# Performance work log

Hardware: AMD Instinct MI355X
Metric: run time of the kernel (lower is better)

The kernel has to match this reference:

```python
import jax, jax.numpy as jnp
import numpy as np

B, L, D = 64, 192, 1024        # batch, tokens (pre_len), in_dim
RES, DIFF, COND = 512, 256, 512
H, DH = 16, 64                 # heads, dim_head; inner = H*DH = 1024
INNER = H * DH
DFF = 4 * D                    # LinearEncoder d_ff
LC = 192                       # cond length


def setup_inputs() -> dict:
    key = jax.random.key(0)
    ks = jax.random.split(key, 16)
    n = lambda k, s, sc=1.0: jax.random.normal(k, s, dtype=jnp.float32) * sc
    return {
        "x": n(ks[0], (B, L, D)),
        "conds": n(ks[1], (B, LC, COND)),
        "diff_emb": n(ks[2], (B, DIFF)),
        "w_diff": n(ks[3], (2 * RES, DIFF), 0.02), "b_diff": jnp.zeros((2 * RES,), jnp.float32),
        "w_cond": n(ks[4], (2 * RES, COND), 0.02), "b_cond": jnp.zeros((2 * RES,), jnp.float32),
        "wq": n(ks[5], (INNER, D), 0.02),
        "wk": n(ks[6], (INNER, 2 * RES), 0.02),
        "wv": n(ks[7], (INNER, 2 * RES), 0.02),
        "wo": n(ks[8], (D, INNER), 0.02), "bo": jnp.zeros((D,), jnp.float32),
        "ln1_g": jnp.ones((D,), jnp.float32), "ln1_b": jnp.zeros((D,), jnp.float32),
        "ln2_g": jnp.ones((D,), jnp.float32), "ln2_b": jnp.zeros((D,), jnp.float32),
        "w_out": n(ks[9], (2 * D, RES), 0.02), "b_out": jnp.zeros((2 * D,), jnp.float32),
        "enc_wv": n(ks[10], (D, D), 0.02), "enc_bv": jnp.zeros((D,), jnp.float32),
        "enc_wo": n(ks[11], (D, D), 0.02), "enc_bo": jnp.zeros((D,), jnp.float32),
        "weight_mat": (jnp.eye(L, dtype=jnp.float32) + jax.random.normal(ks[12], (L, L), dtype=jnp.float32))[None],
        "conv1_w": n(ks[13], (DFF, D), 0.02), "conv1_b": jnp.zeros((DFF,), jnp.float32),
        "conv2_w": n(ks[14], (D, DFF), 0.02), "conv2_b": jnp.zeros((D,), jnp.float32),
        "enc_n1_g": jnp.ones((D,), jnp.float32), "enc_n1_b": jnp.zeros((D,), jnp.float32),
        "enc_n2_g": jnp.ones((D,), jnp.float32), "enc_n2_b": jnp.zeros((D,), jnp.float32),
    }


def _ln(x, g, b):
    m = jnp.mean(x, -1, keepdims=True)
    v = jnp.mean((x - m) ** 2, -1, keepdims=True)
    return (x - m) * jax.lax.rsqrt(v + 1e-5) * g + b


def reference(x, conds, diff_emb, w_diff, b_diff, w_cond, b_cond, wq, wk, wv, wo, bo,
              ln1_g, ln1_b, ln2_g, ln2_b, w_out, b_out, enc_wv, enc_bv, enc_wo, enc_bo,
              weight_mat, conv1_w, conv1_b, conv2_w, conv2_b,
              enc_n1_g, enc_n1_b, enc_n2_g, enc_n2_b):
    res = x
    # diff embedding broadcast-add (permute/unsqueeze in torch == add over token dim)
    x = x + (diff_emb @ w_diff.T + b_diff)[:, None, :]          # [B,L,D]
    # --- LinearEncoder (dropout is identity at inference) ---
    values = x @ enc_wv.T + enc_bv
    A = jax.nn.softplus(weight_mat[0])                          # [L,L]
    A = A / jnp.sum(A, -1, keepdims=True)                       # F.normalize(p=1)
    new_x = jnp.einsum('ij,bjd->bid', A, values)                # token mixing
    x = x + new_x @ enc_wo.T + enc_bo
    x = _ln(x, enc_n1_g, enc_n1_b)
    y = jax.nn.gelu(jnp.einsum('bld,fd->blf', x, conv1_w) + conv1_b, approximate=False)
    y = jnp.einsum('blf,df->bld', y, conv2_w) + conv2_b
    x = _ln(x + y, enc_n2_g, enc_n2_b)
    # --- norm1 + cross attention ---
    x = _ln(x, ln1_g, ln1_b)
    cond = conds @ w_cond.T + b_cond                            # [B,Lc,2*RES]
    b, l = x.shape[0], x.shape[1]
    q = (x @ wq.T).reshape(b, l, H, DH)
    k = (cond @ wk.T).reshape(b, -1, H, DH)
    v = (cond @ wv.T).reshape(b, -1, H, DH)
    scale = DH ** -0.5
    sim = jnp.einsum('bihd,bjhd->bhij', q * scale, k)           # [B,H,L,Lc]
    attn = jax.nn.softmax(sim, axis=-1)
    o = jnp.einsum('bhij,bjhd->bihd', attn, v).reshape(b, l, INNER)
    x = o @ wo.T + bo
    # --- gated residual ---
    x = _ln(x, ln2_g, ln2_b)
    gate, filt = jnp.split(x, 2, axis=2)
    x = jnp.tanh(gate) * jax.nn.sigmoid(filt)                   # [B,L,RES]
    x = x @ w_out.T + b_out                                     # [B,L,2D]
    x = jnp.where(x >= 0, x, 0.4 * x)                           # leaky_relu(0.4)
    out, skip = jnp.split(x, 2, axis=2)
    out = (res + out) / jnp.sqrt(jnp.float32(2.0))
    return out, skip
```

## Files before the change

### kernel.cpp

```cpp
#include <hip/hip_runtime.h>

typedef unsigned short ushort_t;
typedef __attribute__((ext_vector_type(8))) short bf16x8;
typedef __attribute__((ext_vector_type(4))) float f32x4;
typedef __attribute__((ext_vector_type(4))) unsigned short u16x4;

#define DEV __device__ __forceinline__

typedef const __attribute__((address_space(1))) void GV;
typedef __attribute__((address_space(3))) void SV;

DEV void gl_lds16(const ushort_t* g, ushort_t* l) {
    __builtin_amdgcn_global_load_lds((GV*)g, (SV*)l, 16, 0, 0);
}

DEV float bf2f(unsigned short u) {
    union { unsigned u; float f; } c; c.u = ((unsigned)u) << 16; return c.f;
}
DEV unsigned short f2bf(float f) {
    union { float f; unsigned u; } c; c.f = f;
    unsigned u = c.u + 0x7fffu + ((c.u >> 16) & 1u);
    return (unsigned short)(u >> 16);
}

DEV f32x4 mfma32(bf16x8 a, bf16x8 b, f32x4 c) {
    return __builtin_amdgcn_mfma_f32_16x16x32_bf16(a, b, c, 0, 0, 0);
}

#define VMCNT6  asm volatile("s_waitcnt vmcnt(6)" ::: "memory")
#define VMCNT0  asm volatile("s_waitcnt vmcnt(0)" ::: "memory")
#define LGKM0   asm volatile("s_waitcnt lgkmcnt(0)" ::: "memory")
#define SCHEDB  __builtin_amdgcn_sched_barrier(0)
#define BAR     __builtin_amdgcn_s_barrier()

struct CvtSeg { const float* src; ushort_t* dst; };
struct CvtArgs { CvtSeg s[10]; int cum[11]; };

__global__ void cvt_multi(CvtArgs a, int total4) {
    for (int i = blockIdx.x * 256 + threadIdx.x; i < total4; i += gridDim.x * 256) {
        int seg = 0;
        #pragma unroll
        for (int t = 1; t < 10; t++) if (i >= a.cum[t]) seg = t;
        int off = i - a.cum[seg];
        f32x4 v = *(const f32x4*)(a.s[seg].src + (size_t)off * 4);
        u16x4 o;
        #pragma unroll
        for (int j = 0; j < 4; j++) o[j] = f2bf(v[j]);
        *(u16x4*)(a.s[seg].dst + (size_t)off * 4) = o;
    }
}

__global__ void cvt_kernel(const float* __restrict__ in, ushort_t* __restrict__ out, int n4) {
    for (int i = blockIdx.x * 256 + threadIdx.x; i < n4; i += gridDim.x * 256) {
        f32x4 v = *(const f32x4*)(in + (size_t)i * 4);
        u16x4 o;
        #pragma unroll
        for (int j = 0; j < 4; j++) o[j] = f2bf(v[j]);
        *(u16x4*)(out + (size_t)i * 4) = o;
    }
}

__global__ void anorm_kernel(const float* __restrict__ wm, ushort_t* __restrict__ apad) {
    int row = blockIdx.x;
    int lane = threadIdx.x;
    if (row >= 192) {
        apad[row * 192 + lane] = 0;
        apad[row * 192 + lane + 64] = 0;
        apad[row * 192 + lane + 128] = 0;
        return;
    }
    float x0 = wm[row * 192 + lane];
    float x1 = wm[row * 192 + lane + 64];
    float x2 = wm[row * 192 + lane + 128];
    float s0 = (x0 > 20.f) ? x0 : log1pf(expf(x0));
    float s1 = (x1 > 20.f) ? x1 : log1pf(expf(x1));
    float s2 = (x2 > 20.f) ? x2 : log1pf(expf(x2));
    float t = s0 + s1 + s2;
    #pragma unroll
    for (int m = 1; m < 64; m <<= 1) t += __shfl_xor(t, m);
    float inv = 1.f / t;
    apad[row * 192 + lane]       = f2bf(s0 * inv);
    apad[row * 192 + lane + 64]  = f2bf(s1 * inv);
    apad[row * 192 + lane + 128] = f2bf(s2 * inv);
}

__global__ void diffproj_kernel(const float* __restrict__ emb, const float* __restrict__ w,
                                const float* __restrict__ bias, float* __restrict__ out) {
    int id = blockIdx.x * 256 + threadIdx.x;
    int b = id >> 10, n = id & 1023;
    const float* e = emb + b * 256;
    const float* wr = w + (size_t)n * 256;
    float acc = bias[n];
    for (int k2 = 0; k2 < 256; k2++) acc += e[k2] * wr[k2];
    out[id] = acc;
}

__global__ void x1_kernel(const float* __restrict__ x, const float* __restrict__ dp,
                          ushort_t* __restrict__ out) {
    const size_t N4 = 12288ULL * 1024 / 4;
    for (size_t i = (size_t)blockIdx.x * 256 + threadIdx.x; i < N4; i += (size_t)gridDim.x * 256) {
        size_t e = i * 4;
        size_t row = e >> 10;
        int d = (int)(e & 1023);
        int bb = (int)(row / 192);
        f32x4 xv = *(const f32x4*)(x + e);
        u16x4 o4;
        #pragma unroll
        for (int j = 0; j < 4; j++) o4[j] = f2bf(xv[j] + dp[bb * 1024 + d + j]);
        *(u16x4*)(out + e) = o4;
    }
}

__global__ __launch_bounds__(256) void transp_kernel(const ushort_t* __restrict__ in,
                                                     ushort_t* __restrict__ out) {
    __shared__ ushort_t t[32][33];
    int b = blockIdx.z, jt = blockIdx.y, dt = blockIdx.x;
    int tx = threadIdx.x & 31, ty = threadIdx.x >> 5;
    size_t ib = (size_t)b * 192 * 1024;
    #pragma unroll
    for (int i = 0; i < 4; i++) {
        int j = ty + i * 8;
        t[j][tx] = in[ib + (size_t)(jt * 32 + j) * 1024 + dt * 32 + tx];
    }
    __syncthreads();
    size_t ob = (size_t)b * 1024 * 192;
    #pragma unroll
    for (int i = 0; i < 4; i++) {
        int d = ty + i * 8;
        out[ob + (size_t)(dt * 32 + d) * 192 + jt * 32 + tx] = t[tx][d];
    }
}

template<int EPI>
__global__ __launch_bounds__(512, 2) void gemm256(
    const ushort_t* __restrict__ A, int lda, long long sAz,
    const ushort_t* __restrict__ W, int ldw, long long sWz,
    void* __restrict__ Cv, int ldc, long long sCz,
    int Mbound, int K,
    const float* __restrict__ bias,
    const ushort_t* __restrict__ resid,
    float scale,
    const float* __restrict__ resf)
{
    __shared__ ushort_t smem[65536];
    const int tid = threadIdx.x;
    const int wave = tid >> 6, lane = tid & 63, l15 = lane & 15, g = lane >> 4;
    const int wm = wave >> 2, wn = wave & 3;

    int bx = blockIdx.x, by = blockIdx.y;
    if (gridDim.z == 1) {
        int gx = gridDim.x, nwg = gx * gridDim.y;
        if ((nwg & 7) == 0) {
            int orig = by * gx + bx;
            int logi = (orig & 7) * (nwg >> 3) + (orig >> 3);
            bx = logi % gx; by = logi / gx;
        }
    }
    const ushort_t* Ab = A + (size_t)blockIdx.z * sAz + (size_t)by * 256 * lda;
    const ushort_t* Wb = W + (size_t)blockIdx.z * sWz + (size_t)bx * 256 * ldw;

    const int chunkr = lane >> 3;
    const int swsrc  = ((lane & 7) ^ chunkr) * 8;
    const int NT = K >> 6;

    auto SH_A = [&](int tile, int half, int buf) {
        const ushort_t* src = Ab + (size_t)(half * 128) * lda + (tile << 6) + swsrc;
        ushort_t* dst = smem + (buf * 2 + half) * 8192;
        int c = wave * 2;
        gl_lds16(src + (size_t)(c * 8 + chunkr) * lda,       dst + c * 512);
        gl_lds16(src + (size_t)((c + 1) * 8 + chunkr) * lda, dst + (c + 1) * 512);
    };
    auto SH_B = [&](int tile, int half, int buf) {
        const ushort_t* src = Wb + (size_t)(half * 128) * ldw + (tile << 6) + swsrc;
        ushort_t* dst = smem + 32768 + (buf * 2 + half) * 8192;
        int c = wave * 2;
        gl_lds16(src + (size_t)(c * 8 + chunkr) * ldw,       dst + c * 512);
        gl_lds16(src + (size_t)((c + 1) * 8 + chunkr) * ldw, dst + (c + 1) * 512);
    };

    auto LDA_ = [&](bf16x8 (&aa)[4][2], int half, int buf) {
        const char* base = (const char*)(smem + (buf * 2 + half) * 8192);
        #pragma unroll
        for (int m = 0; m < 4; m++) {
            int r = wm * 64 + m * 16 + l15;
            #pragma unroll
            for (int kk = 0; kk < 2; kk++)
                aa[m][kk] = *(const bf16x8*)(base + r * 128 + ((kk * 64 + g * 16) ^ ((l15 & 7) << 4)));
        }
    };
    auto LDB_ = [&](bf16x8 (&bb)[2][2], int half, int buf) {
        const char* base = (const char*)(smem + 32768 + (buf * 2 + half) * 8192);
        #pragma unroll
        for (int n = 0; n < 2; n++) {
            int r = wn * 32 + n * 16 + l15;
            #pragma unroll
            for (int kk = 0; kk < 2; kk++)
                bb[n][kk] = *(const bf16x8*)(base + r * 128 + ((kk * 64 + g * 16) ^ ((l15 & 7) << 4)));
        }
    };

    f32x4 acc[2][2][4][2] = {};
    bf16x8 afr[4][2], blo[2][2], bhi[2][2];

    auto MM = [&](f32x4 (&aq)[4][2], bf16x8 (&bb)[2][2]) {
        #pragma unroll
        for (int m = 0; m < 4; m++)
            #pragma unroll
            for (int n = 0; n < 2; n++)
                #pragma unroll
                for (int kk = 0; kk < 2; kk++)
                    aq[m][n] = mfma32(afr[m][kk], bb[n][kk], aq[m][n]);
    };

    SH_A(0, 0, 0); SH_B(0, 1, 0); SH_A(0, 1, 0); SH_B(0, 0, 0);
    {
        int t1 = (NT > 1) ? 1 : 0;
        SH_A(t1, 0, 1); SH_B(t1, 1, 1); SH_A(t1, 1, 1);
    }
    VMCNT6;
    BAR;

    for (int t = 0; t < NT; t++) {
        const int b = t & 1, nb = b ^ 1;
        const int t1 = (t + 1 < NT) ? t + 1 : NT - 1;
        const int t2 = (t + 2 < NT) ? t + 2 : NT - 1;
        LDA_(afr, 0, b); LDB_(blo, 0, b);
        SH_B(t1, 0, nb);
        BAR; LGKM0; SCHEDB;
        __builtin_amdgcn_s_setprio(1); MM(acc[0][0], blo); __builtin_amdgcn_s_setprio(0);
        BAR;
        LDB_(bhi, 1, b);
        SH_A(t2, 0, b);
        BAR; LGKM0; SCHEDB;
        __builtin_amdgcn_s_setprio(1); MM(acc[0][1], bhi); __builtin_amdgcn_s_setprio(0);
        BAR;
        LDA_(afr, 1, b);
        SH_B(t2, 1, b);
        BAR; LGKM0; SCHEDB;
        __builtin_amdgcn_s_setprio(1); MM(acc[1][1], bhi); __builtin_amdgcn_s_setprio(0);
        BAR;
        SH_A(t2, 1, b);
        VMCNT6;
        BAR; SCHEDB;
        __builtin_amdgcn_s_setprio(1); MM(acc[1][0], blo); __builtin_amdgcn_s_setprio(0);
        BAR;
    }
    VMCNT0;

    #pragma unroll
    for (int mh = 0; mh < 2; mh++)
    #pragma unroll
    for (int nh = 0; nh < 2; nh++)
    #pragma unroll
    for (int m = 0; m < 4; m++)
    #pragma unroll
    for (int n = 0; n < 2; n++) {
        int Cc = bx * 256 + nh * 128 + wn * 32 + n * 16 + l15;
        float bval = 0.f;
        if (EPI == 1 || EPI == 2 || EPI == 3 || EPI == 5) bval = bias[Cc];
        #pragma unroll
        for (int q = 0; q < 4; q++) {
            int R = by * 256 + mh * 128 + wm * 64 + m * 16 + g * 4 + q;
            if (R < Mbound) {
                float t = acc[mh][nh][m][n][q];
                if (EPI == 5) {
                    t += bval;
                    t = (t >= 0.f) ? t : 0.4f * t;
                    float* Of = (float*)Cv;
                    if (Cc < 1024)
                        Of[(size_t)R * 1024 + Cc] = (resf[(size_t)R * 1024 + Cc] + t) * 0.70710678118654752f;
                    else
                        Of[12582912ULL + (size_t)R * 1024 + (Cc - 1024)] = t;
                } else {
                    ushort_t* Co = (ushort_t*)Cv + (size_t)blockIdx.z * sCz;
                    if (EPI == 1) t += bval;
                    if (EPI == 2) { t += bval; t = 0.5f * t * (1.f + erff(t * 0.70710678118654752f)); }
                    if (EPI == 3) { t += bval + bf2f(resid[(size_t)R * ldc + Cc]); }
                    if (EPI == 4) { t *= scale; }
                    Co[(size_t)R * ldc + Cc] = f2bf(t);
                }
            }
        }
    }
}

DEV void red2(float& a, float& b) {
    #pragma unroll
    for (int m = 1; m < 64; m <<= 1) { a += __shfl_xor(a, m); b += __shfl_xor(b, m); }
    __shared__ float sa[4], sb[4];
    int w = threadIdx.x >> 6;
    __syncthreads();
    if ((threadIdx.x & 63) == 0) { sa[w] = a; sb[w] = b; }
    __syncthreads();
    a = sa[0] + sa[1] + sa[2] + sa[3];
    b = sb[0] + sb[1] + sb[2] + sb[3];
}

__global__ __launch_bounds__(256) void ln_kernel(const ushort_t* __restrict__ in,
                                                 const float* __restrict__ gg, const float* __restrict__ bb,
                                                 ushort_t* __restrict__ out) {
    size_t row = blockIdx.x;
    int c0 = threadIdx.x * 4;
    u16x4 r4 = *(const u16x4*)(in + row * 1024 + c0);
    float x[4];
    float s = 0.f, sq = 0.f;
    #pragma unroll
    for (int j = 0; j < 4; j++) { x[j] = bf2f(r4[j]); s += x[j]; sq += x[j] * x[j]; }
    red2(s, sq);
    float m = s * (1.f / 1024.f);
    float var = sq * (1.f / 1024.f) - m * m;
    float rs = rsqrtf(var + 1e-5f);
    u16x4 o4;
    #pragma unroll
    for (int j = 0; j < 4; j++) o4[j] = f2bf((x[j] - m) * rs * gg[c0 + j] + bb[c0 + j]);
    *(u16x4*)(out + row * 1024 + c0) = o4;
}

__global__ __launch_bounds__(256) void ln2_kernel(const ushort_t* __restrict__ in,
                                                  const float* __restrict__ g1, const float* __restrict__ b1,
                                                  const float* __restrict__ g2, const float* __restrict__ b2,
                                                  ushort_t* __restrict__ out) {
    size_t row = blockIdx.x;
    int c0 = threadIdx.x * 4;
    u16x4 r4 = *(const u16x4*)(in + row * 1024 + c0);
    float x[4];
    float s = 0.f, sq = 0.f;
    #pragma unroll
    for (int j = 0; j < 4; j++) { x[j] = bf2f(r4[j]); s += x[j]; sq += x[j] * x[j]; }
    red2(s, sq);
    float m = s * (1.f / 1024.f);
    float var = sq * (1.f / 1024.f) - m * m;
    float rs = rsqrtf(var + 1e-5f);
    float t[4];
    float s2 = 0.f, sq2 = 0.f;
    #pragma unroll
    for (int j = 0; j < 4; j++) {
        t[j] = (x[j] - m) * rs * g1[c0 + j] + b1[c0 + j];
        s2 += t[j]; sq2 += t[j] * t[j];
    }
    red2(s2, sq2);
    float m2 = s2 * (1.f / 1024.f);
    float var2 = sq2 * (1.f / 1024.f) - m2 * m2;
    float rs2 = rsqrtf(var2 + 1e-5f);
    u16x4 o4;
    #pragma unroll
    for (int j = 0; j < 4; j++) o4[j] = f2bf((t[j] - m2) * rs2 * g2[c0 + j] + b2[c0 + j]);
    *(u16x4*)(out + row * 1024 + c0) = o4;
}

__global__ __launch_bounds__(256) void lngate_kernel(const ushort_t* __restrict__ in,
                                                     const float* __restrict__ gg, const float* __restrict__ bb,
                                                     ushort_t* __restrict__ out) {
    __shared__ float buf[1024];
    size_t row = blockIdx.x;
    int c0 = threadIdx.x * 4;
    u16x4 r4 = *(const u16x4*)(in + row * 1024 + c0);
    float x[4];
    float s = 0.f, sq = 0.f;
    #pragma unroll
    for (int j = 0; j < 4; j++) { x[j] = bf2f(r4[j]); s += x[j]; sq += x[j] * x[j]; }
    red2(s, sq);
    float m = s * (1.f / 1024.f);
    float var = sq * (1.f / 1024.f) - m * m;
    float rs = rsqrtf(var + 1e-5f);
    #pragma unroll
    for (int j = 0; j < 4; j++) buf[c0 + j] = (x[j] - m) * rs * gg[c0 + j] + bb[c0 + j];
    __syncthreads();
    if (threadIdx.x < 128) {
        int c = threadIdx.x * 4;
        u16x4 o4;
        #pragma unroll
        for (int j = 0; j < 4; j++) {
            float gv = buf[c + j], fv = buf[c + j + 512];
            o4[j] = f2bf(tanhf(gv) * (1.f / (1.f + expf(-fv))));
        }
        *(u16x4*)(out + row * 512 + c) = o4;
    }
}

__global__ __launch_bounds__(256) void attn_kernel(const ushort_t* __restrict__ q,
                                                   const ushort_t* __restrict__ k,
                                                   const ushort_t* __restrict__ v,
                                                   ushort_t* __restrict__ o, int ldkv) {
    __shared__ ushort_t vT[64][208];
    __shared__ ushort_t pS[4][16][208];
    const int tid = threadIdx.x, wave = tid >> 6, lane = tid & 63, l15 = lane & 15, g = lane >> 4;
    const int qb = blockIdx.x, h = blockIdx.y, b = blockIdx.z;
    const size_t baseq = (size_t)b * 192 * 1024 + h * 64;
    const size_t basekv = (size_t)b * 192 * ldkv + h * 64;
    #pragma unroll
    for (int it = 0; it < 6; ++it) {
        int idx = it * 256 + tid;
        int j = idx >> 3, d8 = (idx & 7) * 8;
        bf16x8 vv = *(const bf16x8*)(v + basekv + (size_t)j * ldkv + d8);
        #pragma unroll
        for (int e = 0; e < 8; e++) vT[d8 + e][j] = (ushort_t)vv[e];
    }
    const int qrow = qb * 64 + wave * 16 + l15;
    bf16x8 aq[2];
    #pragma unroll
    for (int kk = 0; kk < 2; kk++)
        aq[kk] = *(const bf16x8*)(q + baseq + (size_t)qrow * 1024 + kk * 32 + g * 8);
    f32x4 s[12] = {};
    #pragma unroll
    for (int ni = 0; ni < 12; ni++) {
        #pragma unroll
        for (int kk = 0; kk < 2; kk++) {
            bf16x8 bk = *(const bf16x8*)(k + basekv + (size_t)(ni * 16 + l15) * ldkv + kk * 32 + g * 8);
            s[ni] = mfma32(aq[kk], bk, s[ni]);
        }
    }
    float sminv[4];
    #pragma unroll
    for (int qq = 0; qq < 4; qq++) {
        float m = s[0][qq];
        #pragma unroll
        for (int ni = 1; ni < 12; ni++) m = fmaxf(m, s[ni][qq]);
        #pragma unroll
        for (int msk = 1; msk < 16; msk <<= 1) m = fmaxf(m, __shfl_xor(m, msk));
        float sum = 0.f;
        #pragma unroll
        for (int ni = 0; ni < 12; ni++) {
            float p = expf(s[ni][qq] - m);
            s[ni][qq] = p;
            sum += p;
        }
        #pragma unroll
        for (int msk = 1; msk < 16; msk <<= 1) sum += __shfl_xor(sum, msk);
        sminv[qq] = 1.f / sum;
    }
    #pragma unroll
    for (int ni = 0; ni < 12; ni++)
        #pragma unroll
        for (int qq = 0; qq < 4; qq++)
            pS[wave][g * 4 + qq][ni * 16 + l15] = f2bf(s[ni][qq]);
    __syncthreads();
    f32x4 oa[4] = {};
    #pragma unroll
    for (int ks = 0; ks < 6; ks++) {
        bf16x8 pa = *(const bf16x8*)(&pS[wave][l15][ks * 32 + g * 8]);
        #pragma unroll
        for (int di = 0; di < 4; di++) {
            bf16x8 bv = *(const bf16x8*)(&vT[di * 16 + l15][ks * 32 + g * 8]);
            oa[di] = mfma32(pa, bv, oa[di]);
        }
    }
    #pragma unroll
    for (int di = 0; di < 4; di++)
        #pragma unroll
        for (int qq = 0; qq < 4; qq++) {
            int row = qb * 64 + wave * 16 + g * 4 + qq;
            o[(size_t)b * 192 * 1024 + (size_t)row * 1024 + h * 64 + di * 16 + l15] =
                f2bf(oa[di][qq] * sminv[qq]);
        }
}

extern "C" void kernel_launch(void* const* d_in, const int* in_sizes, int n_in,
                              void* d_out, int out_size, void* d_ws, size_t ws_size,
                              hipStream_t stream) {
    (void)in_sizes; (void)n_in; (void)out_size; (void)ws_size;
    const float* x_f     = (const float*)d_in[0];
    const float* conds   = (const float*)d_in[1];
    const float* demb    = (const float*)d_in[2];
    const float* w_diff  = (const float*)d_in[3];
    const float* b_diff  = (const float*)d_in[4];
    const float* w_cond  = (const float*)d_in[5];
    const float* b_cond  = (const float*)d_in[6];
    const float* wq      = (const float*)d_in[7];
    const float* wk      = (const float*)d_in[8];
    const float* wv      = (const float*)d_in[9];
    const float* wo      = (const float*)d_in[10];
    const float* bo      = (const float*)d_in[11];
    const float* ln1_g   = (const float*)d_in[12];
    const float* ln1_b   = (const float*)d_in[13];
    const float* ln2_g   = (const float*)d_in[14];
    const float* ln2_b   = (const float*)d_in[15];
    const float* w_out   = (const float*)d_in[16];
    const float* b_out   = (const float*)d_in[17];
    const float* enc_wv  = (const float*)d_in[18];
    const float* enc_bv  = (const float*)d_in[19];
    const float* enc_wo  = (const float*)d_in[20];
    const float* enc_bo  = (const float*)d_in[21];
    const float* wmat    = (const float*)d_in[22];
    const float* conv1_w = (const float*)d_in[23];
    const float* conv1_b = (const float*)d_in[24];
    const float* conv2_w = (const float*)d_in[25];
    const float* conv2_b = (const float*)d_in[26];
    const float* en1_g   = (const float*)d_in[27];
    const float* en1_b   = (const float*)d_in[28];
    const float* en2_g   = (const float*)d_in[29];
    const float* en2_b   = (const float*)d_in[30];

    char* ws = (char*)d_ws;
    size_t off = 0;
    auto nxt = [&](size_t b) { size_t r = off; off += (b + 255) & ~(size_t)255; return r; };

    const size_t RB = 12288ULL * 1024 * 2;
    size_t o_wencv = nxt(1048576 * 2);
    size_t o_wenco = nxt(1048576 * 2);
    size_t o_conv1 = nxt(4194304 * 2);
    size_t o_conv2 = nxt(4194304 * 2);
    size_t o_wq    = nxt(1048576 * 2);
    size_t o_wkv   = nxt(2097152 * 2);
    size_t o_wo    = nxt(1048576 * 2);
    size_t o_wcond = nxt(524288 * 2);
    size_t o_wout  = nxt(1048576 * 2);
    size_t o_apad  = nxt(256 * 192 * 2);
    size_t o_dp    = nxt(64 * 1024 * 4);
    size_t o_R     = nxt(8 * RB);

    auto WS = [&](size_t o_) { return (ushort_t*)(ws + o_); };
    auto R  = [&](int i)     { return (ushort_t*)(ws + o_R + (size_t)i * RB); };

    {
        CvtArgs ca;
        const float* srcs[10] = { enc_wv, enc_wo, conv1_w, conv2_w, wq, wk, wv, wo, w_cond, w_out };
        ushort_t*    dsts[10] = { WS(o_wencv), WS(o_wenco), WS(o_conv1), WS(o_conv2), WS(o_wq),
                                  WS(o_wkv), WS(o_wkv) + 1048576, WS(o_wo), WS(o_wcond), WS(o_wout) };
        int          n4s[10]  = { 262144, 262144, 1048576, 1048576, 262144,
                                  262144, 262144, 262144, 131072, 262144 };
        int cum = 0;
        for (int i = 0; i < 10; i++) { ca.s[i].src = srcs[i]; ca.s[i].dst = dsts[i]; ca.cum[i] = cum; cum += n4s[i]; }
        ca.cum[10] = cum;
        cvt_multi<<<dim3(1024), dim3(256), 0, stream>>>(ca, cum);
    }

    anorm_kernel<<<dim3(256), dim3(64), 0, stream>>>(wmat, WS(o_apad));
    diffproj_kernel<<<dim3(256), dim3(256), 0, stream>>>(demb, w_diff, b_diff, (float*)(ws + o_dp));
    x1_kernel<<<dim3(3072), dim3(256), 0, stream>>>(x_f, (const float*)(ws + o_dp), R(0));

    gemm256<1><<<dim3(4, 48, 1), 512, 0, stream>>>(R(0), 1024, 0, WS(o_wencv), 1024, 0,
        R(1), 1024, 0, 12288, 1024, enc_bv, nullptr, 0.f, nullptr);
    transp_kernel<<<dim3(32, 6, 64), 256, 0, stream>>>(R(1), R(2));
    gemm256<0><<<dim3(4, 1, 64), 512, 0, stream>>>(WS(o_apad), 192, 0, R(2), 192, 196608LL,
        R(3), 1024, 196608LL, 192, 192, nullptr, nullptr, 0.f, nullptr);
    gemm256<3><<<dim3(4, 48, 1), 512, 0, stream>>>(R(3), 1024, 0, WS(o_wenco), 1024, 0,
        R(4), 1024, 0, 12288, 1024, enc_bo, R(0), 0.f, nullptr);
    ln_kernel<<<dim3(12288), 256, 0, stream>>>(R(4), en1_g, en1_b, R(5));
    gemm256<2><<<dim3(16, 48, 1), 512, 0, stream>>>(R(5), 1024, 0, WS(o_conv1), 1024, 0,
        R(0), 4096, 0, 12288, 1024, conv1_b, nullptr, 0.f, nullptr);
    gemm256<3><<<dim3(4, 48, 1), 512, 0, stream>>>(R(0), 4096, 0, WS(o_conv2), 4096, 0,
        R(6), 1024, 0, 12288, 4096, conv2_b, R(5), 0.f, nullptr);
    ln2_kernel<<<dim3(12288), 256, 0, stream>>>(R(6), en2_g, en2_b, ln1_g, ln1_b, R(7));
    gemm256<4><<<dim3(4, 48, 1), 512, 0, stream>>>(R(7), 1024, 0, WS(o_wq), 1024, 0,
        R(0), 1024, 0, 12288, 1024, nullptr, nullptr, 0.125f, nullptr);
    cvt_kernel<<<dim3(512), dim3(256), 0, stream>>>(conds, R(4), 6291456 / 4);
    gemm256<1><<<dim3(4, 48, 1), 512, 0, stream>>>(R(4), 512, 0, WS(o_wcond), 512, 0,
        R(5), 1024, 0, 12288, 512, b_cond, nullptr, 0.f, nullptr);
    gemm256<0><<<dim3(8, 48, 1), 512, 0, stream>>>(R(5), 1024, 0, WS(o_wkv), 1024, 0,
        R(1), 2048, 0, 12288, 1024, nullptr, nullptr, 0.f, nullptr);
    attn_kernel<<<dim3(3, 16, 64), 256, 0, stream>>>(R(0), R(1), R(1) + 1024, R(3), 2048);
    gemm256<1><<<dim3(4, 48, 1), 512, 0, stream>>>(R(3), 1024, 0, WS(o_wo), 1024, 0,
        R(6), 1024, 0, 12288, 1024, bo, nullptr, 0.f, nullptr);
    lngate_kernel<<<dim3(12288), 256, 0, stream>>>(R(6), ln2_g, ln2_b, R(4));
    gemm256<5><<<dim3(8, 48, 1), 512, 0, stream>>>(R(4), 512, 0, WS(o_wout), 512, 0,
        d_out, 1024, 0, 12288, 512, b_out, nullptr, 0.f, x_f);
}
```

Measured before the change: 1.129 ms.

## Double-buffer LDS fragments in register and prefetch next A tile during MFMA

```diff
diff --git a/kernel.cpp b/kernel.cpp
--- a/kernel.cpp
+++ b/kernel.cpp
@@ -30,7 +30,6 @@
 #define VMCNT6  asm volatile("s_waitcnt vmcnt(6)" ::: "memory")
 #define VMCNT0  asm volatile("s_waitcnt vmcnt(0)" ::: "memory")
 #define LGKM0   asm volatile("s_waitcnt lgkmcnt(0)" ::: "memory")
-#define SCHEDB  __builtin_amdgcn_sched_barrier(0)
 #define BAR     __builtin_amdgcn_s_barrier()
 
 struct CvtSeg { const float* src; ushort_t* dst; };
@@ -200,16 +199,18 @@
     };
 
     f32x4 acc[2][2][4][2] = {};
-    bf16x8 afr[4][2], blo[2][2], bhi[2][2];
-
-    auto MM = [&](f32x4 (&aq)[4][2], bf16x8 (&bb)[2][2]) {
+    bf16x8 a0[4][2], a1[4][2], b0[2][2], b1[2][2];
+
+    auto MMQ = [&](f32x4 (&aq)[4][2], bf16x8 (&aa)[4][2], bf16x8 (&bb)[2][2]) {
+        __builtin_amdgcn_s_setprio(1);
         #pragma unroll
         for (int m = 0; m < 4; m++)
             #pragma unroll
             for (int n = 0; n < 2; n++)
                 #pragma unroll
                 for (int kk = 0; kk < 2; kk++)
-                    aq[m][n] = mfma32(afr[m][kk], bb[n][kk], aq[m][n]);
+                    aq[m][n] = mfma32(aa[m][kk], bb[n][kk], aq[m][n]);
+        __builtin_amdgcn_s_setprio(0);
     };
 
     SH_A(0, 0, 0); SH_B(0, 1, 0); SH_A(0, 1, 0); SH_B(0, 0, 0);
@@ -219,33 +220,32 @@
     }
     VMCNT6;
     BAR;
+    LDA_(a0, 0, 0);
 
     for (int t = 0; t < NT; t++) {
         const int b = t & 1, nb = b ^ 1;
         const int t1 = (t + 1 < NT) ? t + 1 : NT - 1;
         const int t2 = (t + 2 < NT) ? t + 2 : NT - 1;
-        LDA_(afr, 0, b); LDB_(blo, 0, b);
+        LDB_(b0, 0, b); LDB_(b1, 1, b);
         SH_B(t1, 0, nb);
-        BAR; LGKM0; SCHEDB;
-        __builtin_amdgcn_s_setprio(1); MM(acc[0][0], blo); __builtin_amdgcn_s_setprio(0);
+        MMQ(acc[0][0], a0, b0);
         BAR;
-        LDB_(bhi, 1, b);
+        LDA_(a1, 1, b);
         SH_A(t2, 0, b);
-        BAR; LGKM0; SCHEDB;
-        __builtin_amdgcn_s_setprio(1); MM(acc[0][1], bhi); __builtin_amdgcn_s_setprio(0);
+        MMQ(acc[0][1], a0, b1);
         BAR;
-        LDA_(afr, 1, b);
         SH_B(t2, 1, b);
-        BAR; LGKM0; SCHEDB;
-        __builtin_amdgcn_s_setprio(1); MM(acc[1][1], bhi); __builtin_amdgcn_s_setprio(0);
+        MMQ(acc[1][1], a1, b1);
         BAR;
         SH_A(t2, 1, b);
         VMCNT6;
-        BAR; SCHEDB;
-        __builtin_amdgcn_s_setprio(1); MM(acc[1][0], blo); __builtin_amdgcn_s_setprio(0);
         BAR;
+        LDA_(a0, 0, nb);
+        MMQ(acc[1][0], a1, b0);
+        BAR;
     }
     VMCNT0;
+    LGKM0;
 
     #pragma unroll
     for (int mh = 0; mh < 2; mh++)
```

After: 1.102 ms. 1.02x faster.
